# Performance work log

Measured on AMD Instinct MI355X. Metric: run time of the kernel, lower is better.

Reference implementation:

```python
import jax, jax.numpy as jnp
from jax import lax
import numpy as np

B, N, C, P = 8, 512, 256, 7
CQ = C // 4
NMS_THRESH = 0.5
BBOX_XFORM_CLIP = 4.135166556742356  # log(1000/16)


def setup_inputs():
    key = jax.random.key(0)
    ks = jax.random.split(key, 24)
    rn = lambda k, s, sc=0.02: jax.random.normal(k, s, jnp.float32) * sc
    box_feats_q = jax.random.normal(ks[0], (B, N, C, P, P), jnp.float32)
    box_feats_s = jax.random.normal(ks[1], (B, 1, C, P, P), jnp.float32)
    xy = jax.random.uniform(ks[2], (B, N, 2), jnp.float32, 0.0, 700.0)
    wh = jax.random.uniform(ks[3], (B, N, 2), jnp.float32, 8.0, 96.0)
    proposals = jnp.concatenate([xy, xy + wh], axis=-1)  # [B,N,4] valid x1y1x2y2
    image_size = jnp.array([800, 800], jnp.int32)  # (H, W)
    return {
        'box_feats_q': box_feats_q, 'box_feats_s': box_feats_s,
        'proposals': proposals, 'image_size': image_size,
        'W1': rn(ks[4], (CQ, 2 * C)),          # conv1 1x1: 2C -> C/4
        'W2': rn(ks[5], (CQ, CQ, 3, 3)),       # conv2 3x3 valid
        'W3': rn(ks[6], (C, CQ)),              # conv3 1x1: C/4 -> C
        'Wcor': rn(ks[7], (C, C)),             # conv_cor 1x1
        'fc1_w': rn(ks[8], (C, 2 * C)), 'fc1_b': jnp.zeros((C,), jnp.float32),
        'fc2_w': rn(ks[9], (C, C)), 'fc2_b': jnp.zeros((C,), jnp.float32),
        'sfc_w': rn(ks[10], (1, C)), 'sfc_b': jnp.zeros((1,), jnp.float32),
        'scor_w': rn(ks[11], (1, C)), 'scor_b': jnp.zeros((1,), jnp.float32),
        'spr_w': rn(ks[12], (1, C)), 'spr_b': jnp.zeros((1,), jnp.float32),
        'dpr_w': rn(ks[13], (4, C)), 'dpr_b': jnp.zeros((4,), jnp.float32),
    }


def avgpool3(x):  # AvgPool2d(3, stride=1), NCHW
    s = lax.reduce_window(x, 0.0, lax.add, (1, 1, 3, 3), (1, 1, 1, 1), 'VALID')
    return s / 9.0


def head_forward(box_feats_q, box_feats_s, W1, W2, W3, Wcor, fc1_w, fc1_b, fc2_w,
                 fc2_b, sfc_w, sfc_b, scor_w, scor_b, spr_w, spr_b, dpr_w, dpr_b):
    M = B * N
    x_q = box_feats_q.reshape(M, C, P, P)
    x_s = jnp.broadcast_to(box_feats_s, (B, N, C, P, P)).reshape(M, C, P, P)
    # FC branch (avgpool_fc == global mean over 7x7)
    x_fc = jnp.concatenate([x_q.mean((2, 3)), x_s.mean((2, 3))], axis=1)  # [M,2C]
    h = jax.nn.relu(x_fc @ fc1_w.T + fc1_b)
    h = jax.nn.relu(h @ fc2_w.T + fc2_b)
    score_fc = h @ sfc_w.T + sfc_b  # [M,1]
    # Correlation branch: grouped 7x7 conv == per-channel spatial dot product
    x_cor_q = jnp.einsum('oc,mchw->mohw', Wcor, x_q)
    x_cor_s = jnp.einsum('oc,mchw->mohw', Wcor, x_s)
    x_relu = jax.nn.relu((x_cor_q * x_cor_s).sum((2, 3)))  # [M,C]
    score_cor = x_relu @ scor_w.T + scor_b  # [M,1]
    # Conv branch
    x = jnp.concatenate([x_q, x_s], axis=1)                    # [M,2C,7,7]
    x = jax.nn.relu(jnp.einsum('oc,mchw->mohw', W1, x))        # [M,CQ,7,7]
    x = avgpool3(x)                                            # [M,CQ,5,5]
    x = jax.nn.relu(lax.conv_general_dilated(x, W2, (1, 1), 'VALID',
        dimension_numbers=('NCHW', 'OIHW', 'NCHW')))           # [M,CQ,3,3]
    x = jax.nn.relu(jnp.einsum('oc,mchw->mohw', W3, x))        # [M,C,3,3]
    x = avgpool3(x).squeeze(3).squeeze(2)                      # [M,C]
    score_pr = x @ spr_w.T + spr_b
    pred_scores = score_pr + score_cor + score_fc              # [M,1]
    pred_deltas = x @ dpr_w.T + dpr_b                          # [M,4]
    return pred_scores, pred_deltas


def decode_boxes(deltas, boxes):
    w = boxes[:, 2] - boxes[:, 0]
    h = boxes[:, 3] - boxes[:, 1]
    cx = boxes[:, 0] + 0.5 * w
    cy = boxes[:, 1] + 0.5 * h
    dx, dy = deltas[:, 0], deltas[:, 1]
    dw = jnp.minimum(deltas[:, 2], BBOX_XFORM_CLIP)
    dh = jnp.minimum(deltas[:, 3], BBOX_XFORM_CLIP)
    pcx, pcy = dx * w + cx, dy * h + cy
    pw, ph = jnp.exp(dw) * w, jnp.exp(dh) * h
    return jnp.stack([pcx - 0.5 * pw, pcy - 0.5 * ph,
                      pcx + 0.5 * pw, pcy + 0.5 * ph], axis=1)


def nms_mask(boxes, scores, thresh):  # fixed-shape NMS -> keep mask [n]
    n = boxes.shape[0]
    order = jnp.argsort(-scores)
    b = boxes[order]
    area = jnp.maximum(b[:, 2] - b[:, 0], 0) * jnp.maximum(b[:, 3] - b[:, 1], 0)
    idx = jnp.arange(n)

    def body(i, keep):
        x1 = jnp.maximum(b[i, 0], b[:, 0]); y1 = jnp.maximum(b[i, 1], b[:, 1])
        x2 = jnp.minimum(b[i, 2], b[:, 2]); y2 = jnp.minimum(b[i, 3], b[:, 3])
        inter = jnp.maximum(x2 - x1, 0) * jnp.maximum(y2 - y1, 0)
        iou = inter / jnp.maximum(area[i] + area - inter, 1e-9)
        suppress = (iou > thresh) & (idx > i) & keep[i]
        return keep & ~suppress

    keep_sorted = lax.fori_loop(0, n, body, jnp.ones((n,), bool))
    return jnp.zeros((n,), bool).at[order].set(keep_sorted)


def reference(box_feats_q, box_feats_s, proposals, image_size, W1, W2, W3, Wcor,
              fc1_w, fc1_b, fc2_w, fc2_b, sfc_w, sfc_b, scor_w, scor_b,
              spr_w, spr_b, dpr_w, dpr_b):
    pred_scores, pred_deltas = head_forward(
        box_feats_q, box_feats_s, W1, W2, W3, Wcor, fc1_w, fc1_b, fc2_w, fc2_b,
        sfc_w, sfc_b, scor_w, scor_b, spr_w, spr_b, dpr_w, dpr_b)
    M = B * N
    # decode on detached deltas
    pred_boxes = decode_boxes(lax.stop_gradient(pred_deltas), proposals.reshape(M, 4))
    H = image_size[0].astype(jnp.float32)
    W_ = image_size[1].astype(jnp.float32)
    pred_boxes = jnp.stack([
        jnp.clip(pred_boxes[:, 0], 0.0, W_), jnp.clip(pred_boxes[:, 1], 0.0, H),
        jnp.clip(pred_boxes[:, 2], 0.0, W_), jnp.clip(pred_boxes[:, 3], 0.0, H)],
        axis=1).reshape(B, N, 4)
    scores = jax.nn.sigmoid(lax.stop_gradient(pred_scores)).reshape(B, N)
    keep = jax.vmap(lambda bx, sc: nms_mask(bx, sc, NMS_THRESH))(pred_boxes, scores)
    # boxes/scores padded to fixed [B,N,...]; keep mask marks NMS survivors
    return pred_boxes, scores, keep
```

## Files before the change

### kernel.cpp

```cpp
#include <hip/hip_runtime.h>
#include <math.h>

typedef float f4 __attribute__((ext_vector_type(4)));
typedef f4 f4u __attribute__((aligned(4)));
typedef float f32x4 __attribute__((ext_vector_type(4)));
typedef short short8 __attribute__((ext_vector_type(8)));

constexpr int NB  = 8;
constexpr int NN  = 512;
constexpr int NC  = 256;
constexpr int NHW = 49;
constexpr int NM  = NB * NN;
constexpr int XS  = 260;

constexpr size_t WS_SMEAN = 0;
constexpr size_t WS_YST   = 2048;
constexpr size_t WS_UST   = 102400;
constexpr size_t WS_WFH   = 127488;
constexpr size_t WS_WFL   = 168448;
constexpr size_t WS_SP    = 209408;
constexpr size_t WS_QMEAN = 213504;
constexpr size_t WS_W2FH  = 1262080;
constexpr size_t WS_W2FL  = 1280512;
constexpr size_t WS_NEED_BIG = 1298944;

constexpr size_t OUT_SCORES = (size_t)NM * 4;
constexpr size_t OUT_KEEP   = OUT_SCORES + NM;

__device__ __forceinline__ float block_reduce_sum(float v, float* red) {
    int t = threadIdx.x;
#pragma unroll
    for (int off = 32; off > 0; off >>= 1) v += __shfl_down(v, off, 64);
    __syncthreads();
    if ((t & 63) == 0) red[t >> 6] = v;
    __syncthreads();
    return red[0] + red[1] + red[2] + red[3];
}

__device__ __forceinline__ unsigned short bf16_rne(float f) {
    unsigned u = __float_as_uint(f);
    return (unsigned short)((u + 0x7FFFu + ((u >> 16) & 1u)) >> 16);
}
__device__ __forceinline__ float bf16_to_f(unsigned short h) {
    return __uint_as_float(((unsigned)h) << 16);
}

__device__ __forceinline__ void stage_xT(const float* __restrict__ g, float* sx, int t) {
#pragma unroll
    for (int rep = 0; rep < 13; ++rep) {
        int id = rep * 256 + t;
        if (id < 3136) {
            int c4 = id / 49;
            int hw = id - c4 * 49;
            f4 v;
            v[0] = g[(c4 * 4 + 0) * 49 + hw];
            v[1] = g[(c4 * 4 + 1) * 49 + hw];
            v[2] = g[(c4 * 4 + 2) * 49 + hw];
            v[3] = g[(c4 * 4 + 3) * 49 + hw];
            *(f4*)&sx[hw * XS + c4 * 4] = v;
        }
    }
}

__global__ __launch_bounds__(256, 2) void k_prep(
    const float* __restrict__ bfs, const float* __restrict__ Wcor,
    const float* __restrict__ W1, const float* __restrict__ W2,
    float* __restrict__ ws, int use_mfma_conv)
{
    int t = threadIdx.x, blk = blockIdx.x;

    if (blk >= 104) {
        if (!use_mfma_conv) return;
        int ks2 = blk - 104;
        int mt = t >> 6, l = t & 63;
        int row = mt * 16 + (l & 15);
        int kk0 = ks2 * 32 + (l >> 4) * 8;
        const float* src = W2 + (size_t)row * 576 + kk0;
        short* dh = (short*)(ws + WS_W2FH) + ((size_t)(mt * 18 + ks2) * 64 + l) * 8;
        short* dl = (short*)(ws + WS_W2FL) + ((size_t)(mt * 18 + ks2) * 64 + l) * 8;
#pragma unroll
        for (int j = 0; j < 8; ++j) {
            float v = src[j];
            unsigned short hh = bf16_rne(v);
            dh[j] = (short)hh;
            dl[j] = (short)bf16_rne(v - bf16_to_f(hh));
        }
        return;
    }

    if (blk >= 64) {
        int ob = (blk - 64) * 4 + (t >> 6);
        int l = t & 63;
        int mt = ob >> 3, ks = ob & 7;
        int row = mt * 16 + (l & 15);
        int k0 = ks * 32 + (l >> 4) * 8;
        const float* src = (row < 256) ? (Wcor + (size_t)row * 256 + k0)
                                       : (W1 + (size_t)(row - 256) * 512 + k0);
        short hv[8], lv[8];
#pragma unroll
        for (int j = 0; j < 8; ++j) {
            float v = src[j];
            unsigned short hh = bf16_rne(v);
            unsigned short hl = bf16_rne(v - bf16_to_f(hh));
            hv[j] = (short)hh; lv[j] = (short)hl;
        }
        short* dh = (short*)(ws + WS_WFH) + ((size_t)ob * 64 + l) * 8;
        short* dl = (short*)(ws + WS_WFL) + ((size_t)ob * 64 + l) * 8;
#pragma unroll
        for (int j = 0; j < 8; ++j) { dh[j] = hv[j]; dl[j] = lv[j]; }
        return;
    }

    __shared__ __align__(16) float smem[49 * XS + 16];
    float* sx = smem;
    int b = blk >> 3;
    int og8 = blk & 7;

    stage_xT(bfs + (size_t)b * 12544, sx, t);
    __syncthreads();

    if (og8 == 0) {
        float s = 0.f;
        for (int hw = 0; hw < 49; ++hw) s += sx[hw * XS + t];
        ws[WS_SMEAN + (size_t)b * 256 + t] = s * (1.f / 49.f);
    }

    int og2 = t >> 3, hwg = t & 7;
    int hwb = (hwg == 7) ? 0 : hwg * 7;
    int oA = og8 * 32 + og2;
    bool do_u = (og8 < 2);
    int o2 = og8 * 32 + og2;

    float acc0[7] = {0,0,0,0,0,0,0};
    float a1a[7]  = {0,0,0,0,0,0,0};
    const float* xrow = sx + hwb * XS;
    const float* w0r = Wcor + (size_t)oA * 256;
    const float* war = W1 + (size_t)o2 * 512 + 256;

#pragma unroll 1
    for (int c4 = 0; c4 < 64; ++c4) {
        f4 xv[7];
#pragma unroll
        for (int i = 0; i < 7; ++i) xv[i] = *(const f4*)&xrow[i * XS + c4 * 4];
        f4 w0 = *(const f4*)&w0r[c4 * 4];
        f4 wa = *(const f4*)&war[c4 * 4];
#pragma unroll
        for (int j = 0; j < 4; ++j) {
#pragma unroll
            for (int i = 0; i < 7; ++i) {
                float x = xv[i][j];
                acc0[i] = fmaf(w0[j], x, acc0[i]);
                a1a[i]  = fmaf(wa[j], x, a1a[i]);
            }
        }
    }

    if (hwg < 7) {
#pragma unroll
        for (int i = 0; i < 7; ++i) {
            int hw = hwb + i;
            ws[WS_YST + ((size_t)b * 256 + oA) * 49 + hw] = acc0[i];
            if (do_u)
                ws[WS_UST + ((size_t)b * 64 + o2) * 49 + hw] = a1a[i];
        }
    }
}

__global__ __launch_bounds__(256, 3) void k_heavy(
    const float* __restrict__ bfq,
    const float* __restrict__ W2, const float* __restrict__ W3,
    const float* __restrict__ scor_w, const float* __restrict__ scor_b,
    const float* __restrict__ spr_w, const float* __restrict__ spr_b,
    const float* __restrict__ dpr_w, const float* __restrict__ dpr_b,
    const float* __restrict__ proposals, const int* __restrict__ image_size,
    float* __restrict__ ws, float* __restrict__ out, int use_mfma_conv)
{
    __shared__ __align__(16) short xh[49 * 256];
    __shared__ __align__(16) short xl[49 * 256];
    __shared__ float red[20];

    int t = threadIdx.x, m = blockIdx.x, b = m >> 9;
    const float* xg = bfq + (size_t)m * 12544 + (size_t)t * 49;

    {
        float qs = 0.f;
#pragma unroll
        for (int r = 0; r < 12; ++r) {
            f4u v = *(const f4u*)&xg[r * 4];
#pragma unroll
            for (int j = 0; j < 4; ++j) {
                int hw = r * 4 + j;
                float x = v[j];
                qs += x;
                unsigned short hh = bf16_rne(x);
                int idx = (hw * 256 + t) ^ ((hw & 7) << 3);
                xh[idx] = (short)hh;
                xl[idx] = (short)bf16_rne(x - bf16_to_f(hh));
            }
        }
        float x48 = xg[48];
        qs += x48;
        unsigned short hh48 = bf16_rne(x48);
        xh[48 * 256 + t] = (short)hh48;
        xl[48 * 256 + t] = (short)bf16_rne(x48 - bf16_to_f(hh48));
        ws[WS_QMEAN + (size_t)m * 256 + t] = qs * (1.f / 49.f);
    }
    __syncthreads();

    int w = t >> 6, l = t & 63, cl = l & 15, g = l >> 4;

    f32x4 acc[5][4];
#pragma unroll
    for (int i = 0; i < 5; ++i)
#pragma unroll
        for (int nt = 0; nt < 4; ++nt) acc[i][nt] = (f32x4)0.f;

    const short* wfH = (const short*)(ws + WS_WFH);
    const short* wfL = (const short*)(ws + WS_WFL);

    int bcol[4];
#pragma unroll
    for (int nt = 0; nt < 4; ++nt) {
        int col = nt * 16 + cl;
        if (col >= 49) col = 0;
        bcol[nt] = col;
    }

#pragma unroll 1
    for (int ks = 0; ks < 8; ++ks) {
        short8 bh[4], bl[4];
#pragma unroll
        for (int nt = 0; nt < 4; ++nt) {
            int col = bcol[nt];
            int idx = (col * 256 + ks * 32 + g * 8) ^ ((col & 7) << 3);
            bh[nt] = *(const short8*)&xh[idx];
            bl[nt] = *(const short8*)&xl[idx];
        }
#pragma unroll
        for (int i = 0; i < 5; ++i) {
            int mt = w + 4 * i;
            size_t off = ((size_t)(mt * 8 + ks) * 64 + l) * 8;
            short8 ah = *(const short8*)&wfH[off];
            short8 al = *(const short8*)&wfL[off];
            acc[i][0] = __builtin_amdgcn_mfma_f32_16x16x32_bf16(ah, bh[0], acc[i][0], 0, 0, 0);
            acc[i][1] = __builtin_amdgcn_mfma_f32_16x16x32_bf16(ah, bh[1], acc[i][1], 0, 0, 0);
            acc[i][2] = __builtin_amdgcn_mfma_f32_16x16x32_bf16(ah, bh[2], acc[i][2], 0, 0, 0);
            acc[i][3] = __builtin_amdgcn_mfma_f32_16x16x32_bf16(ah, bh[3], acc[i][3], 0, 0, 0);
            acc[i][0] = __builtin_amdgcn_mfma_f32_16x16x32_bf16(ah, bl[0], acc[i][0], 0, 0, 0);
            acc[i][1] = __builtin_amdgcn_mfma_f32_16x16x32_bf16(ah, bl[1], acc[i][1], 0, 0, 0);
            acc[i][2] = __builtin_amdgcn_mfma_f32_16x16x32_bf16(ah, bl[2], acc[i][2], 0, 0, 0);
            acc[i][3] = __builtin_amdgcn_mfma_f32_16x16x32_bf16(ah, bl[3], acc[i][3], 0, 0, 0);
            acc[i][0] = __builtin_amdgcn_mfma_f32_16x16x32_bf16(al, bh[0], acc[i][0], 0, 0, 0);
            acc[i][1] = __builtin_amdgcn_mfma_f32_16x16x32_bf16(al, bh[1], acc[i][1], 0, 0, 0);
            acc[i][2] = __builtin_amdgcn_mfma_f32_16x16x32_bf16(al, bh[2], acc[i][2], 0, 0, 0);
            acc[i][3] = __builtin_amdgcn_mfma_f32_16x16x32_bf16(al, bh[3], acc[i][3], 0, 0, 0);
        }
    }

    float csum = 0.f;
    {
        const float* yb = ws + WS_YST + (size_t)b * 256 * 49;
#pragma unroll
        for (int i = 0; i < 4; ++i) {
            int row0 = (w + 4 * i) * 16 + g * 4;
#pragma unroll
            for (int q = 0; q < 4; ++q) {
                int row = row0 + q;
                float p = 0.f;
#pragma unroll
                for (int nt = 0; nt < 4; ++nt) {
                    int col = nt * 16 + cl;
                    if (col < 49) p += acc[i][nt][q] * yb[(size_t)row * 49 + col];
                }
                p += __shfl_xor(p, 1, 64);
                p += __shfl_xor(p, 2, 64);
                p += __shfl_xor(p, 4, 64);
                p += __shfl_xor(p, 8, 64);
                if (cl == 0) csum += fmaxf(p, 0.f) * scor_w[row];
            }
        }
    }
    __syncthreads();

    float* s1    = (float*)xh;
    float* sp1   = s1 + 64 * 52;
    float* sc2T  = s1 + 5120;
    float* cpart = (float*)xl;

    {
        const float* ub = ws + WS_UST + (size_t)b * 64 * 49;
        int ch0 = w * 16 + g * 4;
#pragma unroll
        for (int q = 0; q < 4; ++q) {
            int ch = ch0 + q;
#pragma unroll
            for (int nt = 0; nt < 4; ++nt) {
                int col = nt * 16 + cl;
                if (col < 49)
                    s1[ch * 52 + col] = fmaxf(acc[4][nt][q] + ub[(size_t)ch * 49 + col], 0.f);
            }
        }
    }
    __syncthreads();

    for (int i = t; i < 64 * 25; i += 256) {
        int ch = i / 25, pos = i - ch * 25;
        int py = pos / 5, px = pos - py * 5;
        const float* base = s1 + ch * 52 + py * 7 + px;
        float s = base[0] + base[1] + base[2]
                + base[7] + base[8] + base[9]
                + base[14] + base[15] + base[16];
        sp1[ch * 28 + pos] = s * (1.f / 9.f);
    }
    __syncthreads();

    if (use_mfma_conv) {
        short* bimh = (short*)xl;
        short* biml = ((short*)xl) + 5184;
#pragma unroll 1
        for (int kk = t; kk < 576; kk += 256) {
            int ic = kk / 9;
            int k  = kk - ic * 9;
            int ky = k / 3, kx = k - ky * 3;
            const float* bsp = sp1 + ic * 28 + ky * 5 + kx;
#pragma unroll
            for (int py = 0; py < 3; ++py)
#pragma unroll
                for (int px = 0; px < 3; ++px) {
                    int pos = py * 3 + px;
                    float v = bsp[py * 5 + px];
                    unsigned short hh = bf16_rne(v);
                    int idx = pos * 576 + (kk ^ ((pos & 7) << 3));
                    bimh[idx] = (short)hh;
                    biml[idx] = (short)bf16_rne(v - bf16_to_f(hh));
                }
        }
        __syncthreads();

        f32x4 a2 = (f32x4)0.f;
        const short* w2h = (const short*)(ws + WS_W2FH);
        const short* w2l = (const short*)(ws + WS_W2FL);
        int c9 = (cl < 9) ? cl : 0;
        int bbase = c9 * 576, bxor = (c9 & 7) << 3;
#pragma unroll 1
        for (int ks2 = 0; ks2 < 18; ++ks2) {
            int bidx = bbase + ((ks2 * 32 + g * 8) ^ bxor);
            short8 bh = *(const short8*)&bimh[bidx];
            short8 bl = *(const short8*)&biml[bidx];
            size_t off = ((size_t)(w * 18 + ks2) * 64 + l) * 8;
            short8 ah = *(const short8*)&w2h[off];
            short8 al = *(const short8*)&w2l[off];
            a2 = __builtin_amdgcn_mfma_f32_16x16x32_bf16(ah, bh, a2, 0, 0, 0);
            a2 = __builtin_amdgcn_mfma_f32_16x16x32_bf16(ah, bl, a2, 0, 0, 0);
            a2 = __builtin_amdgcn_mfma_f32_16x16x32_bf16(al, bh, a2, 0, 0, 0);
        }
        if (cl < 9) {
#pragma unroll
            for (int q = 0; q < 4; ++q)
                sc2T[cl * 64 + (w * 16 + g * 4 + q)] = fmaxf(a2[q], 0.f);
        }
        __syncthreads();
    } else {
        {
            int oc = t & 63, icq = t >> 6;
            float a9[9] = {0,0,0,0,0,0,0,0,0};
            const float* wb2 = W2 + (size_t)oc * 576 + icq * 16 * 9;
#pragma unroll 1
            for (int ic16 = 0; ic16 < 16; ++ic16) {
                int ic = icq * 16 + ic16;
                const f4* ar = (const f4*)(sp1 + ic * 28);
                float av[28];
                *(f4*)&av[0]  = ar[0];
                *(f4*)&av[4]  = ar[1];
                *(f4*)&av[8]  = ar[2];
                *(f4*)&av[12] = ar[3];
                *(f4*)&av[16] = ar[4];
                *(f4*)&av[20] = ar[5];
                *(f4*)&av[24] = ar[6];
                const float* wi = wb2 + ic16 * 9;
                f4u w0 = *(const f4u*)wi;
                f4u w1 = *(const f4u*)(wi + 4);
                float wv[9] = { w0[0], w0[1], w0[2], w0[3], w1[0], w1[1], w1[2], w1[3], wi[8] };
#pragma unroll
                for (int py = 0; py < 3; ++py)
#pragma unroll
                    for (int px = 0; px < 3; ++px) {
                        int p9 = py * 3 + px;
#pragma unroll
                        for (int ky = 0; ky < 3; ++ky)
#pragma unroll
                            for (int kx = 0; kx < 3; ++kx)
                                a9[p9] = fmaf(wv[ky * 3 + kx],
                                              av[(py + ky) * 5 + (px + kx)], a9[p9]);
                    }
            }
#pragma unroll
            for (int p = 0; p < 9; ++p)
                cpart[((size_t)(t >> 6) * 64 + (t & 63)) * 11 + p] = a9[p];
        }
        __syncthreads();
        for (int i = t; i < 576; i += 256) {
            int pos = i >> 6, occ = i & 63;
            float s = cpart[((size_t)0 * 64 + occ) * 11 + pos]
                    + cpart[((size_t)1 * 64 + occ) * 11 + pos]
                    + cpart[((size_t)2 * 64 + occ) * 11 + pos]
                    + cpart[((size_t)3 * 64 + occ) * 11 + pos];
            sc2T[pos * 64 + occ] = fmaxf(s, 0.f);
        }
        __syncthreads();
    }

    float xfin;
    {
        float xw[9] = {0,0,0,0,0,0,0,0,0};
        const f4* wr = (const f4*)(W3 + (size_t)t * 64);
#pragma unroll 1
        for (int gg = 0; gg < 16; ++gg) {
            f4 wv4 = wr[gg];
#pragma unroll
            for (int p = 0; p < 9; ++p) {
                f4 c = *(const f4*)(sc2T + p * 64 + gg * 4);
                xw[p] = fmaf(wv4[0], c[0], xw[p]);
                xw[p] = fmaf(wv4[1], c[1], xw[p]);
                xw[p] = fmaf(wv4[2], c[2], xw[p]);
                xw[p] = fmaf(wv4[3], c[3], xw[p]);
            }
        }
        float s = 0.f;
#pragma unroll
        for (int p = 0; p < 9; ++p) s += fmaxf(xw[p], 0.f);
        xfin = s * (1.f / 9.f);
    }

    float v0 = xfin * spr_w[t] + csum;
    float v1 = xfin * dpr_w[0 * 256 + t];
    float v2 = xfin * dpr_w[1 * 256 + t];
    float v3 = xfin * dpr_w[2 * 256 + t];
    float v4 = xfin * dpr_w[3 * 256 + t];
#pragma unroll
    for (int off = 32; off > 0; off >>= 1) {
        v0 += __shfl_xor(v0, off, 64);
        v1 += __shfl_xor(v1, off, 64);
        v2 += __shfl_xor(v2, off, 64);
        v3 += __shfl_xor(v3, off, 64);
        v4 += __shfl_xor(v4, off, 64);
    }
    if (l == 0) {
        red[w * 5 + 0] = v0; red[w * 5 + 1] = v1; red[w * 5 + 2] = v2;
        red[w * 5 + 3] = v3; red[w * 5 + 4] = v4;
    }
    __syncthreads();

    if (t == 0) {
        float r_s  = red[0] + red[5] + red[10] + red[15];
        float r_d0 = red[1] + red[6] + red[11] + red[16];
        float r_d1 = red[2] + red[7] + red[12] + red[17];
        float r_d2 = red[3] + red[8] + red[13] + red[18];
        float r_d3 = red[4] + red[9] + red[14] + red[19];

        ws[WS_SP + m] = r_s + spr_b[0] + scor_b[0];

        float d0 = r_d0 + dpr_b[0];
        float d1 = r_d1 + dpr_b[1];
        float d2 = fminf(r_d2 + dpr_b[2], 4.135166556742356f);
        float d3 = fminf(r_d3 + dpr_b[3], 4.135166556742356f);

        const float* pr = proposals + (size_t)m * 4;
        float x1p = pr[0], y1p = pr[1], x2p = pr[2], y2p = pr[3];
        float wd = x2p - x1p, hd = y2p - y1p;
        float cx = x1p + 0.5f * wd, cy = y1p + 0.5f * hd;
        float pcx = d0 * wd + cx, pcy = d1 * hd + cy;
        float pw = expf(d2) * wd, ph = expf(d3) * hd;
        float Wf = (float)image_size[1];
        float Hf = (float)image_size[0];
        out[(size_t)m * 4 + 0] = fminf(fmaxf(pcx - 0.5f * pw, 0.f), Wf);
        out[(size_t)m * 4 + 1] = fminf(fmaxf(pcy - 0.5f * ph, 0.f), Hf);
        out[(size_t)m * 4 + 2] = fminf(fmaxf(pcx + 0.5f * pw, 0.f), Wf);
        out[(size_t)m * 4 + 3] = fminf(fmaxf(pcy + 0.5f * ph, 0.f), Hf);
    }
}

__global__ __launch_bounds__(256) void k_fc(
    const float* __restrict__ fc1_w, const float* __restrict__ fc1_b,
    const float* __restrict__ fc2_w, const float* __restrict__ fc2_b,
    const float* __restrict__ sfc_w, const float* __restrict__ sfc_b,
    float* __restrict__ ws, float* __restrict__ out)
{
    __shared__ __align__(16) float sxfc[16][512];
    __shared__ __align__(16) float sh1[16][256];
    __shared__ float s_red[64];
    int t = threadIdx.x;
    int m0 = blockIdx.x * 16;
    int w = t >> 6, l = t & 63;

#pragma unroll
    for (int mi = 0; mi < 16; ++mi) {
        int mg = m0 + mi;
        int b = mg >> 9;
        sxfc[mi][t]       = ws[WS_QMEAN + (size_t)mg * 256 + t];
        sxfc[mi][256 + t] = ws[WS_SMEAN + (size_t)b * 256 + t];
    }
    __syncthreads();

    {
        const f4* wr = (const f4*)(fc1_w + t * 512);
        float acc[16];
#pragma unroll
        for (int mi = 0; mi < 16; ++mi) acc[mi] = 0.f;
#pragma unroll 1
        for (int k4 = 0; k4 < 128; ++k4) {
            f4 wv = wr[k4];
#pragma unroll
            for (int mi = 0; mi < 16; ++mi) {
                f4 x = ((const f4*)sxfc[mi])[k4];
                acc[mi] = fmaf(wv[0], x[0], acc[mi]);
                acc[mi] = fmaf(wv[1], x[1], acc[mi]);
                acc[mi] = fmaf(wv[2], x[2], acc[mi]);
                acc[mi] = fmaf(wv[3], x[3], acc[mi]);
            }
        }
        float bb = fc1_b[t];
#pragma unroll
        for (int mi = 0; mi < 16; ++mi) sh1[mi][t] = fmaxf(acc[mi] + bb, 0.f);
    }
    __syncthreads();

    float val[16];
    {
        const f4* wr = (const f4*)(fc2_w + t * 256);
        float acc[16];
#pragma unroll
        for (int mi = 0; mi < 16; ++mi) acc[mi] = 0.f;
#pragma unroll 1
        for (int k4 = 0; k4 < 64; ++k4) {
            f4 wv = wr[k4];
#pragma unroll
            for (int mi = 0; mi < 16; ++mi) {
                f4 x = ((const f4*)sh1[mi])[k4];
                acc[mi] = fmaf(wv[0], x[0], acc[mi]);
                acc[mi] = fmaf(wv[1], x[1], acc[mi]);
                acc[mi] = fmaf(wv[2], x[2], acc[mi]);
                acc[mi] = fmaf(wv[3], x[3], acc[mi]);
            }
        }
        float bb = fc2_b[t];
        float sw = sfc_w[t];
#pragma unroll
        for (int mi = 0; mi < 16; ++mi) val[mi] = sw * fmaxf(acc[mi] + bb, 0.f);
    }

#pragma unroll
    for (int mi = 0; mi < 16; ++mi) {
        float v = val[mi];
#pragma unroll
        for (int off = 32; off > 0; off >>= 1) v += __shfl_xor(v, off, 64);
        if (l == 0) s_red[w * 16 + mi] = v;
    }
    __syncthreads();

    if (t < 16) {
        float r = s_red[0 * 16 + t] + s_red[1 * 16 + t]
                + s_red[2 * 16 + t] + s_red[3 * 16 + t];
        float tot = ws[WS_SP + m0 + t] + (r + sfc_b[0]);
        out[OUT_SCORES + m0 + t] = 1.0f / (1.0f + expf(-tot));
    }
}

__global__ __launch_bounds__(1024) void k_nms(float* __restrict__ out)
{
    __shared__ float ssc[512];
    __shared__ __align__(16) float sbox[512 * 4];
    __shared__ float sarea[512];
    __shared__ int   sidx[512];
    __shared__ unsigned long long smask[512 * 8];

    int t = threadIdx.x, b = blockIdx.x;
    int wv = t >> 6, lane = t & 63;
    const float* sc_g = out + OUT_SCORES + (size_t)b * 512;

    if (t < 512) ssc[t] = sc_g[t];
    __syncthreads();

    if (t < 512) {
        float si = ssc[t];
        int r = 0;
        for (int j = 0; j < 512; ++j) {
            float sj = ssc[j];
            r += (int)((sj > si) || (sj == si && j < t));
        }
        f4 v = *(const f4*)(out + ((size_t)b * 512 + t) * 4);
        *(f4*)&sbox[r * 4] = v;
        sarea[r] = fmaxf(v[2] - v[0], 0.f) * fmaxf(v[3] - v[1], 0.f);
        sidx[r] = t;
    }
    __syncthreads();

#pragma unroll 1
    for (int k = 0; k < 32; ++k) {
        int i = wv * 32 + k;
        f4 bi = *(const f4*)&sbox[i * 4];
        float ai = sarea[i];
#pragma unroll
        for (int w8 = 0; w8 < 8; ++w8) {
            int j = w8 * 64 + lane;
            f4 bj = *(const f4*)&sbox[j * 4];
            float aj = sarea[j];
            float xx1 = fmaxf(bi[0], bj[0]), yy1 = fmaxf(bi[1], bj[1]);
            float xx2 = fminf(bi[2], bj[2]), yy2 = fminf(bi[3], bj[3]);
            float inter = fmaxf(xx2 - xx1, 0.f) * fmaxf(yy2 - yy1, 0.f);
            float iou = inter / fmaxf(ai + aj - inter, 1e-9f);
            bool sup = (iou > 0.5f) && (j > i);
            unsigned long long bal = __ballot(sup);
            if (lane == 0) smask[i * 8 + w8] = bal;
        }
    }
    __syncthreads();

    if (wv == 0) {
        unsigned long long kw = ~0ull;
        unsigned long long nxt = (lane < 8) ? smask[lane] : 0ull;
        for (int i = 0; i < 512; ++i) {
            unsigned long long cur = nxt;
            if (i < 511 && lane < 8) nxt = smask[(size_t)(i + 1) * 8 + lane];
            unsigned long long wi = __shfl(kw, i >> 6, 64);
            if ((wi >> (i & 63)) & 1ull) {
                if (lane < 8) kw &= ~cur;
            }
        }
        if (lane < 8) smask[lane] = kw;
    }
    __syncthreads();

    if (t < 512) {
        unsigned long long word = smask[t >> 6];
        out[OUT_KEEP + (size_t)b * 512 + sidx[t]] =
            ((word >> (t & 63)) & 1ull) ? 1.0f : 0.0f;
    }
}

extern "C" void kernel_launch(void* const* d_in, const int* in_sizes, int n_in,
                              void* d_out, int out_size, void* d_ws, size_t ws_size,
                              hipStream_t stream) {
    const float* bfq       = (const float*)d_in[0];
    const float* bfs       = (const float*)d_in[1];
    const float* proposals = (const float*)d_in[2];
    const int*   image_sz  = (const int*)d_in[3];
    const float* W1        = (const float*)d_in[4];
    const float* W2        = (const float*)d_in[5];
    const float* W3        = (const float*)d_in[6];
    const float* Wcor      = (const float*)d_in[7];
    const float* fc1_w     = (const float*)d_in[8];
    const float* fc1_b     = (const float*)d_in[9];
    const float* fc2_w     = (const float*)d_in[10];
    const float* fc2_b     = (const float*)d_in[11];
    const float* sfc_w     = (const float*)d_in[12];
    const float* sfc_b     = (const float*)d_in[13];
    const float* scor_w    = (const float*)d_in[14];
    const float* scor_b    = (const float*)d_in[15];
    const float* spr_w     = (const float*)d_in[16];
    const float* spr_b     = (const float*)d_in[17];
    const float* dpr_w     = (const float*)d_in[18];
    const float* dpr_b     = (const float*)d_in[19];
    float* out = (float*)d_out;
    float* ws  = (float*)d_ws;

    int big = (ws_size >= WS_NEED_BIG * sizeof(float)) ? 1 : 0;

    k_prep<<<big ? 122 : 104, 256, 0, stream>>>(bfs, Wcor, W1, W2, ws, big);
    k_heavy<<<NM, 256, 0, stream>>>(bfq, W2, W3,
                                    scor_w, scor_b, spr_w, spr_b,
                                    dpr_w, dpr_b, proposals, image_sz, ws, out, big);
    k_fc<<<NM / 16, 256, 0, stream>>>(fc1_w, fc1_b, fc2_w, fc2_b,
                                      sfc_w, sfc_b, ws, out);
    k_nms<<<NB, 1024, 0, stream>>>(out);
}
```

Before: 448.1 us.

## Move FC head to split-bf16 MFMA and pad conv im2col stride

Adds a k_fc_mfma kernel that computes fc1 and fc2 with bf16 hi/lo split MFMA (three products per step), using weight fragments prebuilt by new k_prep blocks. The old VALU FC kernel is kept as a fallback when the workspace is too small. It also changes the im2col row stride in k_heavy from 576 to 584 to reduce LDS bank conflicts. Whether it runs depends on the workspace size check, and the split-bf16 path drops the lo*lo term, which slightly changes precision.

```diff
diff --git a/kernel.cpp b/kernel.cpp
--- a/kernel.cpp
+++ b/kernel.cpp
@@ -23,19 +23,14 @@
 constexpr size_t WS_W2FH  = 1262080;
 constexpr size_t WS_W2FL  = 1280512;
 constexpr size_t WS_NEED_BIG = 1298944;
+constexpr size_t WS_F1H   = 1298944;
+constexpr size_t WS_F1L   = 1364480;
+constexpr size_t WS_F2H   = 1430016;
+constexpr size_t WS_F2L   = 1462784;
+constexpr size_t WS_NEED_BIG2 = 1495552;
 
 constexpr size_t OUT_SCORES = (size_t)NM * 4;
 constexpr size_t OUT_KEEP   = OUT_SCORES + NM;
-
-__device__ __forceinline__ float block_reduce_sum(float v, float* red) {
-    int t = threadIdx.x;
-#pragma unroll
-    for (int off = 32; off > 0; off >>= 1) v += __shfl_down(v, off, 64);
-    __syncthreads();
-    if ((t & 63) == 0) red[t >> 6] = v;
-    __syncthreads();
-    return red[0] + red[1] + red[2] + red[3];
-}
 
 __device__ __forceinline__ unsigned short bf16_rne(float f) {
     unsigned u = __float_as_uint(f);
@@ -62,32 +57,62 @@
     }
 }
 
+__device__ __forceinline__ void build_frag(
+    const float* __restrict__ src, short* __restrict__ dh,
+    short* __restrict__ dl)
+{
+#pragma unroll
+    for (int j = 0; j < 8; ++j) {
+        float v = src[j];
+        unsigned short hh = bf16_rne(v);
+        dh[j] = (short)hh;
+        dl[j] = (short)bf16_rne(v - bf16_to_f(hh));
+    }
+}
+
 __global__ __launch_bounds__(256, 2) void k_prep(
     const float* __restrict__ bfs, const float* __restrict__ Wcor,
     const float* __restrict__ W1, const float* __restrict__ W2,
-    float* __restrict__ ws, int use_mfma_conv)
+    const float* __restrict__ fc1_w, const float* __restrict__ fc2_w,
+    float* __restrict__ ws, int big, int big2)
 {
     int t = threadIdx.x, blk = blockIdx.x;
 
+    if (blk >= 186) {
+        if (!big2) return;
+        int fb = (blk - 186) * 4 + (t >> 6);
+        int l = t & 63;
+        int mt = fb >> 3, ks = fb & 7;
+        int row = mt * 16 + (l & 15);
+        int k0 = ks * 32 + (l >> 4) * 8;
+        build_frag(fc2_w + (size_t)row * 256 + k0,
+                   (short*)(ws + WS_F2H) + ((size_t)fb * 64 + l) * 8,
+                   (short*)(ws + WS_F2L) + ((size_t)fb * 64 + l) * 8);
+        return;
+    }
+    if (blk >= 122) {
+        if (!big2) return;
+        int fb = (blk - 122) * 4 + (t >> 6);
+        int l = t & 63;
+        int mt = fb >> 4, ks = fb & 15;
+        int row = mt * 16 + (l & 15);
+        int k0 = ks * 32 + (l >> 4) * 8;
+        build_frag(fc1_w + (size_t)row * 512 + k0,
+                   (short*)(ws + WS_F1H) + ((size_t)fb * 64 + l) * 8,
+                   (short*)(ws + WS_F1L) + ((size_t)fb * 64 + l) * 8);
+        return;
+    }
     if (blk >= 104) {
-        if (!use_mfma_conv) return;
+        if (!big) return;
         int ks2 = blk - 104;
         int mt = t >> 6, l = t & 63;
         int row = mt * 16 + (l & 15);
         int kk0 = ks2 * 32 + (l >> 4) * 8;
-        const float* src = W2 + (size_t)row * 576 + kk0;
-        short* dh = (short*)(ws + WS_W2FH) + ((size_t)(mt * 18 + ks2) * 64 + l) * 8;
-        short* dl = (short*)(ws + WS_W2FL) + ((size_t)(mt * 18 + ks2) * 64 + l) * 8;
-#pragma unroll
-        for (int j = 0; j < 8; ++j) {
-            float v = src[j];
-            unsigned short hh = bf16_rne(v);
-            dh[j] = (short)hh;
-            dl[j] = (short)bf16_rne(v - bf16_to_f(hh));
-        }
+        build_frag(W2 + (size_t)row * 576 + kk0,
+                   (short*)(ws + WS_W2FH) + ((size_t)(mt * 18 + ks2) * 64 + l) * 8,
+                   (short*)(ws + WS_W2FL) + ((size_t)(mt * 18 + ks2) * 64 + l) * 8);
         return;
     }
-
     if (blk >= 64) {
         int ob = (blk - 64) * 4 + (t >> 6);
         int l = t & 63;
@@ -96,18 +121,9 @@
         int k0 = ks * 32 + (l >> 4) * 8;
         const float* src = (row < 256) ? (Wcor + (size_t)row * 256 + k0)
                                        : (W1 + (size_t)(row - 256) * 512 + k0);
-        short hv[8], lv[8];
-#pragma unroll
-        for (int j = 0; j < 8; ++j) {
-            float v = src[j];
-            unsigned short hh = bf16_rne(v);
-            unsigned short hl = bf16_rne(v - bf16_to_f(hh));
-            hv[j] = (short)hh; lv[j] = (short)hl;
-        }
-        short* dh = (short*)(ws + WS_WFH) + ((size_t)ob * 64 + l) * 8;
-        short* dl = (short*)(ws + WS_WFL) + ((size_t)ob * 64 + l) * 8;
-#pragma unroll
-        for (int j = 0; j < 8; ++j) { dh[j] = hv[j]; dl[j] = lv[j]; }
+        build_frag(src,
+                   (short*)(ws + WS_WFH) + ((size_t)ob * 64 + l) * 8,
+                   (short*)(ws + WS_WFL) + ((size_t)ob * 64 + l) * 8);
         return;
     }
 
@@ -165,6 +181,8 @@
         }
     }
 }
+
+constexpr int IMR = 584;
 
 __global__ __launch_bounds__(256, 3) void k_heavy(
     const float* __restrict__ bfq,
@@ -316,7 +334,7 @@
 
     if (use_mfma_conv) {
         short* bimh = (short*)xl;
-        short* biml = ((short*)xl) + 5184;
+        short* biml = ((short*)xl) + 9 * IMR;
 #pragma unroll 1
         for (int kk = t; kk < 576; kk += 256) {
             int ic = kk / 9;
@@ -330,7 +348,7 @@
                     int pos = py * 3 + px;
                     float v = bsp[py * 5 + px];
                     unsigned short hh = bf16_rne(v);
-                    int idx = pos * 576 + (kk ^ ((pos & 7) << 3));
+                    int idx = pos * IMR + (kk ^ ((pos & 7) << 3));
                     bimh[idx] = (short)hh;
                     biml[idx] = (short)bf16_rne(v - bf16_to_f(hh));
                 }
@@ -341,7 +359,7 @@
         const short* w2h = (const short*)(ws + WS_W2FH);
         const short* w2l = (const short*)(ws + WS_W2FL);
         int c9 = (cl < 9) ? cl : 0;
-        int bbase = c9 * 576, bxor = (c9 & 7) << 3;
+        int bbase = c9 * IMR, bxor = (c9 & 7) << 3;
 #pragma unroll 1
         for (int ks2 = 0; ks2 < 18; ++ks2) {
             int bidx = bbase + ((ks2 * 32 + g * 8) ^ bxor);
@@ -480,7 +498,121 @@
     }
 }
 
-__global__ __launch_bounds__(256) void k_fc(
+__global__ __launch_bounds__(256) void k_fc_mfma(
+    const float* __restrict__ fc1_b, const float* __restrict__ fc2_b,
+    const float* __restrict__ sfc_w, const float* __restrict__ sfc_b,
+    float* __restrict__ ws, float* __restrict__ out)
+{
+    __shared__ __align__(16) short xbh[16 * 512];
+    __shared__ __align__(16) short xbl[16 * 512];
+    __shared__ __align__(16) short hbh[16 * 256];
+    __shared__ __align__(16) short hbl[16 * 256];
+    __shared__ float sred[4][16];
+
+    int t = threadIdx.x;
+    int m0 = blockIdx.x * 16;
+    int w = t >> 6, l = t & 63, cl = l & 15, g = l >> 4;
+
+    {
+        int mi = t >> 4, kg = t & 15;
+        int mg = m0 + mi, b = mg >> 9;
+        int swz = (mi & 7) << 3;
+        const float* qsrc = ws + WS_QMEAN + (size_t)mg * 256;
+        const float* ssrc = ws + WS_SMEAN + (size_t)b * 256;
+#pragma unroll 1
+        for (int kk = 0; kk < 32; ++kk) {
+            int k = kg * 32 + kk;
+            float v = (k < 256) ? qsrc[k] : ssrc[k - 256];
+            unsigned short hh = bf16_rne(v);
+            int idx = mi * 512 + (k ^ swz);
+            xbh[idx] = (short)hh;
+            xbl[idx] = (short)bf16_rne(v - bf16_to_f(hh));
+        }
+    }
+    __syncthreads();
+
+    const short* f1h = (const short*)(ws + WS_F1H);
+    const short* f1l = (const short*)(ws + WS_F1L);
+    f32x4 a1[4];
+#pragma unroll
+    for (int i = 0; i < 4; ++i) a1[i] = (f32x4)0.f;
+    int bxor = (cl & 7) << 3;
+#pragma unroll 1
+    for (int ks = 0; ks < 16; ++ks) {
+        int bidx = cl * 512 + ((ks * 32 + g * 8) ^ bxor);
+        short8 bh = *(const short8*)&xbh[bidx];
+        short8 bl = *(const short8*)&xbl[bidx];
+#pragma unroll
+        for (int i = 0; i < 4; ++i) {
+            int mt = w * 4 + i;
+            size_t off = ((size_t)(mt * 16 + ks) * 64 + l) * 8;
+            short8 ah = *(const short8*)&f1h[off];
+            short8 al = *(const short8*)&f1l[off];
+            a1[i] = __builtin_amdgcn_mfma_f32_16x16x32_bf16(ah, bh, a1[i], 0, 0, 0);
+            a1[i] = __builtin_amdgcn_mfma_f32_16x16x32_bf16(ah, bl, a1[i], 0, 0, 0);
+            a1[i] = __builtin_amdgcn_mfma_f32_16x16x32_bf16(al, bh, a1[i], 0, 0, 0);
+        }
+    }
+#pragma unroll
+    for (int i = 0; i < 4; ++i) {
+        int ch0 = (w * 4 + i) * 16 + g * 4;
+#pragma unroll
+        for (int q = 0; q < 4; ++q) {
+            int ch = ch0 + q;
+            float h = fmaxf(a1[i][q] + fc1_b[ch], 0.f);
+            unsigned short hh = bf16_rne(h);
+            int idx = cl * 256 + (ch ^ bxor);
+            hbh[idx] = (short)hh;
+            hbl[idx] = (short)bf16_rne(h - bf16_to_f(hh));
+        }
+    }
+    __syncthreads();
+
+    const short* f2h = (const short*)(ws + WS_F2H);
+    const short* f2l = (const short*)(ws + WS_F2L);
+    f32x4 a2[4];
+#pragma unroll
+    for (int i = 0; i < 4; ++i) a2[i] = (f32x4)0.f;
+#pragma unroll 1
+    for (int ks = 0; ks < 8; ++ks) {
+        int bidx = cl * 256 + ((ks * 32 + g * 8) ^ bxor);
+        short8 bh = *(const short8*)&hbh[bidx];
+        short8 bl = *(const short8*)&hbl[bidx];
+#pragma unroll
+        for (int i = 0; i < 4; ++i) {
+            int mt = w * 4 + i;
+            size_t off = ((size_t)(mt * 8 + ks) * 64 + l) * 8;
+            short8 ah = *(const short8*)&f2h[off];
+            short8 al = *(const short8*)&f2l[off];
+            a2[i] = __builtin_amdgcn_mfma_f32_16x16x32_bf16(ah, bh, a2[i], 0, 0, 0);
+            a2[i] = __builtin_amdgcn_mfma_f32_16x16x32_bf16(ah, bl, a2[i], 0, 0, 0);
+            a2[i] = __builtin_amdgcn_mfma_f32_16x16x32_bf16(al, bh, a2[i], 0, 0, 0);
+        }
+    }
+
+    float p = 0.f;
+#pragma unroll
+    for (int i = 0; i < 4; ++i) {
+        int ch0 = (w * 4 + i) * 16 + g * 4;
+#pragma unroll
+        for (int q = 0; q < 4; ++q) {
+            int ch = ch0 + q;
+            p += sfc_w[ch] * fmaxf(a2[i][q] + fc2_b[ch], 0.f);
+        }
+    }
+    p += __shfl_xor(p, 16, 64);
+    p += __shfl_xor(p, 32, 64);
+    if (l < 16) sred[w][l] = p;
+    __syncthreads();
+
+    if (t < 16) {
+        float r = sred[0][t] + sred[1][t] + sred[2][t] + sred[3][t];
+        float tot = ws[WS_SP + m0 + t] + (r + sfc_b[0]);
+        out[OUT_SCORES + m0 + t] = 1.0f / (1.0f + expf(-tot));
+    }
+}
+
+__global__ __launch_bounds__(256) void k_fc_valu(
     const float* __restrict__ fc1_w, const float* __restrict__ fc1_b,
     const float* __restrict__ fc2_w, const float* __restrict__ fc2_b,
     const float* __restrict__ sfc_w, const float* __restrict__ sfc_b,
@@ -664,13 +796,19 @@
     float* out = (float*)d_out;
     float* ws  = (float*)d_ws;
 
-    int big = (ws_size >= WS_NEED_BIG * sizeof(float)) ? 1 : 0;
-
-    k_prep<<<big ? 122 : 104, 256, 0, stream>>>(bfs, Wcor, W1, W2, ws, big);
+    int big  = (ws_size >= WS_NEED_BIG  * sizeof(float)) ? 1 : 0;
+    int big2 = (ws_size >= WS_NEED_BIG2 * sizeof(float)) ? 1 : 0;
+    int grid_prep = big2 ? 218 : (big ? 122 : 104);
+
+    k_prep<<<grid_prep, 256, 0, stream>>>(bfs, Wcor, W1, W2, fc1_w, fc2_w,
+                                          ws, big, big2);
     k_heavy<<<NM, 256, 0, stream>>>(bfq, W2, W3,
                                     scor_w, scor_b, spr_w, spr_b,
                                     dpr_w, dpr_b, proposals, image_sz, ws, out, big);
-    k_fc<<<NM / 16, 256, 0, stream>>>(fc1_w, fc1_b, fc2_w, fc2_b,
-                                      sfc_w, sfc_b, ws, out);
+    if (big2)
+        k_fc_mfma<<<NM / 16, 256, 0, stream>>>(fc1_b, fc2_b, sfc_w, sfc_b, ws, out);
+    else
+        k_fc_valu<<<NM / 16, 256, 0, stream>>>(fc1_w, fc1_b, fc2_w, fc2_b,
+                                               sfc_w, sfc_b, ws, out);
     k_nms<<<NB, 1024, 0, stream>>>(out);
 }
```

Result: faster. 412.5 us, median of 2 (-8.0%).
